# Kernel tuning notes

Hardware: AMD Instinct MI355X
Metric: run time of the kernel (lower is better)

## Reference

```python
import jax, jax.numpy as jnp
import numpy as np

N_MODES = 64


def setup_inputs() -> dict:
    key = jax.random.key(0)
    ks = jax.random.split(key, 5)
    B, L, C, M = 32, 8192, 64, N_MODES
    scale = 1.0 / (C * M)
    return {
        "x": jax.random.normal(ks[0], (B, L, C), dtype=jnp.float32),
        "w_spec_real": jax.random.normal(ks[1], (C, C, M), dtype=jnp.float32) * scale,
        "w_spec_imag": jax.random.normal(ks[2], (C, C, M), dtype=jnp.float32) * scale,
        "pw_weight": jax.random.normal(ks[3], (C, C), dtype=jnp.float32) * (1.0 / np.sqrt(C)),
        "pw_bias": jax.random.normal(ks[4], (C,), dtype=jnp.float32) * 0.01,
    }


def reference(x, w_spec_real, w_spec_imag, pw_weight, pw_bias):
    # x: [B, L, C] -> [B, C, L] (matches torch transpose(1, 2))
    xt = jnp.swapaxes(x, 1, 2)
    L = xt.shape[-1]
    xf = jnp.fft.rfft(xt, axis=-1)            # [B, C, F] complex64, F = L//2 + 1
    F = xf.shape[-1]
    K = min(N_MODES, F)
    W = (w_spec_real + 1j * w_spec_imag).astype(xf.dtype)  # [Cin, Cout, M]
    # Batched replacement of the per-mode loop: [B,Cin,K] x [Cin,Cout,K] -> [B,Cout,K]
    tf_low = jnp.einsum('bik,iok->bok', xf[:, :, :K], W[:, :, :K])
    tf = jnp.zeros_like(xf).at[:, :, :K].set(tf_low)
    x_back = jnp.fft.irfft(tf, n=L, axis=-1)  # [B, C, L] real
    # pointwise conv (kernel_size=1): [Cout,Cin] x [B,Cin,L] + bias
    pw = jnp.einsum('oi,bil->bol', pw_weight, xt) + pw_bias[None, :, None]
    return jnp.swapaxes(x_back + pw, 1, 2)     # [B, L, C]
```

## Files before the change

### kernel.cpp

```cpp
#include <hip/hip_runtime.h>
#include <stdint.h>

#define L_     8192
#define NB     32
#define NC     64
#define SPLITK 16
#define CHUNK  (L_ / SPLITK)
#define SXPAD  520

#define BF_OFF  0
#define XF_OFF  (2u  << 20)
#define XR_OFF  (18u << 20)
#define TF_OFF  (19u << 20)

typedef __bf16 bf16x8 __attribute__((ext_vector_type(8)));
typedef float  f32x4  __attribute__((ext_vector_type(4)));

__device__ __forceinline__ unsigned short f2bf(float f) {
  union { float f; unsigned int i; } v; v.f = f;
  unsigned int r = v.i + 0x7fffu + ((v.i >> 16) & 1u);
  return (unsigned short)(r >> 16);
}
__device__ __forceinline__ f32x4 mfma16(bf16x8 a, bf16x8 b, f32x4 c) {
  return __builtin_amdgcn_mfma_f32_16x16x32_bf16(a, b, c, 0, 0, 0);
}

__global__ __launch_bounds__(256) void k0_bf(unsigned short* __restrict__ Bf) {
  const int e0 = (blockIdx.x * 256 + threadIdx.x) * 4;
  const float W0 = 6.283185307179586f / 8192.0f;
  #pragma unroll
  for (int u = 0; u < 4; ++u) {
    const int e = e0 + u;
    const int j = e >> 13, l = e & 8191, k = j >> 1;
    const float th = (float)((k * l) & 8191) * W0;
    float sv, cv; __sincosf(th, &sv, &cv);
    const float a = (k == 0 ? 1.0f : 2.0f) * (1.0f / 8192.0f);
    Bf[e] = f2bf((j & 1) ? (-a * sv) : (a * cv));
  }
}

__global__ __launch_bounds__(256) void k1_dft(const float* __restrict__ x,
                                              const unsigned short* __restrict__ Bf,
                                              float* __restrict__ XFP) {
  const int b = blockIdx.x >> 4;
  const int p = blockIdx.x & 15;
  const int l0 = p * CHUNK;
  const int t = threadIdx.x;
  const int wv = t >> 6, lane = t & 63, q = lane >> 4, n = lane & 15;
  __shared__ uint32_t sx[NC * SXPAD / 2];
  const float* xb = x + (size_t)b * L_ * NC;

  {
    const int g  = t & 15;
    const int r2 = t >> 4;
    for (int s = 0; s < 16; ++s) {
      const int lrow = s * 32 + 2 * r2;
      const f32x4 u0 = *(const f32x4*)(xb + (size_t)(l0 + lrow) * NC + 4 * g);
      const f32x4 u1 = *(const f32x4*)(xb + (size_t)(l0 + lrow + 1) * NC + 4 * g);
      #pragma unroll
      for (int j = 0; j < 4; ++j) {
        __bf16 pk2[2] = {(__bf16)u0[j], (__bf16)u1[j]};
        sx[(4 * g + j) * (SXPAD / 2) + s * 16 + r2] = __builtin_bit_cast(uint32_t, pk2);
      }
    }
  }
  __syncthreads();

  f32x4 acc[2][4];
  #pragma unroll
  for (int i = 0; i < 2; ++i)
    #pragma unroll
    for (int j = 0; j < 4; ++j) acc[i][j] = (f32x4){0.f, 0.f, 0.f, 0.f};
  const unsigned short* sxu = (const unsigned short*)sx;

  for (int ks = 0; ks < CHUNK; ks += 32) {
    const int lb = ks + q * 8;
    bf16x8 bfr[4];
    #pragma unroll
    for (int nt = 0; nt < 4; ++nt)
      bfr[nt] = *(const bf16x8*)(sxu + (nt * 16 + n) * SXPAD + lb);
    #pragma unroll
    for (int mt = 0; mt < 2; ++mt) {
      const bf16x8 afr = *(const bf16x8*)(Bf + (size_t)(wv * 32 + mt * 16 + n) * L_ + l0 + lb);
      #pragma unroll
      for (int nt = 0; nt < 4; ++nt)
        acc[mt][nt] = mfma16(afr, bfr[nt], acc[mt][nt]);
    }
  }

  float* op = XFP + (size_t)(p * NB + b) * 8192;
  #pragma unroll
  for (int mt = 0; mt < 2; ++mt)
    #pragma unroll
    for (int nt = 0; nt < 4; ++nt)
      #pragma unroll
      for (int r = 0; r < 4; ++r)
        op[(wv * 32 + mt * 16 + q * 4 + r) * 64 + nt * 16 + n] = acc[mt][nt][r];
}

__global__ __launch_bounds__(256) void k1b_red(const f32x4* __restrict__ XFP,
                                               f32x4* __restrict__ XFR) {
  const int idx = blockIdx.x * 256 + threadIdx.x;
  f32x4 s = XFP[idx];
  #pragma unroll
  for (int p = 1; p < SPLITK; ++p) {
    const f32x4 v = XFP[(size_t)p * 65536 + idx];
    s[0] += v[0]; s[1] += v[1]; s[2] += v[2]; s[3] += v[3];
  }
  XFR[idx] = s;
}

__global__ __launch_bounds__(256) void k2_mix(const float* __restrict__ XFR,
                                              const float* __restrict__ wr,
                                              const float* __restrict__ wi,
                                              const float* __restrict__ pww,
                                              uint32_t* __restrict__ tf_stage) {
  const int b = blockIdx.x >> 3;
  const int og = blockIdx.x & 7;
  const int t = threadIdx.x;
  __shared__ float sxr[64 * 65];
  __shared__ float sxi[64 * 65];
  const float* xfb = XFR + (size_t)b * 8192;
  for (int e = t; e < 8192; e += 256) {
    const float s = xfb[e];
    const int j = e >> 6, c = e & 63, m = j >> 1;
    if (j & 1) sxi[c * 65 + m] = s; else sxr[c * 65 + m] = s;
  }
  __syncthreads();
  const int k = t & 63;
  const int wv = t >> 6;
  #pragma unroll
  for (int oo = 0; oo < 2; ++oo) {
    const int o = og * 8 + wv * 2 + oo;
    float ar = 0.f, ai = 0.f;
    #pragma unroll 8
    for (int i = 0; i < 64; ++i) {
      const float xr  = sxr[i * 65 + k];
      const float xi_ = sxi[i * 65 + k];
      const float wrv = wr[(size_t)i * 4096 + o * 64 + k];
      const float wiv = wi[(size_t)i * 4096 + o * 64 + k];
      ar = fmaf(xr, wrv, ar);  ar = fmaf(-xi_, wiv, ar);
      ai = fmaf(xr, wiv, ai);  ai = fmaf(xi_, wrv, ai);
    }
    uint32_t* row = tf_stage + ((size_t)b * 64 + o) * 96;
    row[k] = (uint32_t)f2bf(ar) | ((uint32_t)f2bf(ai) << 16);
    if (k < 32)
      row[64 + k] = (uint32_t)f2bf(pww[o * 64 + 2 * k]) |
                    ((uint32_t)f2bf(pww[o * 64 + 2 * k + 1]) << 16);
  }
}

__global__ __launch_bounds__(256) void k2b_copy(const uint4* __restrict__ src,
                                                uint4* __restrict__ dst) {
  const int idx = blockIdx.x * 256 + threadIdx.x;
  dst[idx] = src[idx];
}

__global__ __launch_bounds__(256) void k3_out(const float* __restrict__ x,
                                              const unsigned short* __restrict__ tf,
                                              const float* __restrict__ bias,
                                              float* __restrict__ out) {
  const int b = blockIdx.x >> 6;
  const int lt = blockIdx.x & 63;
  const int wv = threadIdx.x >> 6;
  const int lane = threadIdx.x & 63;
  const int q = lane >> 4;
  const int n = lane & 15;
  const int l0 = lt * 128 + wv * 32;
  const float* xb = x + (size_t)b * L_ * NC;
  const unsigned short* tfb = tf + (size_t)b * 64 * 192;
  const float W0 = 6.283185307179586f / 8192.0f;
  f32x4 acc[2][4];
  #pragma unroll
  for (int i = 0; i < 2; ++i)
    #pragma unroll
    for (int j = 0; j < 4; ++j) acc[i][j] = (f32x4){0.f, 0.f, 0.f, 0.f};
  const int la  = l0 + n;
  const int lb2 = l0 + 16 + n;
  #pragma unroll
  for (int s = 0; s < 6; ++s) {
    const int k0 = s * 32;
    bf16x8 a0, a1;
    if (s < 4) {
      #pragma unroll
      for (int jj = 0; jj < 4; ++jj) {
        const int kf = (k0 >> 1) + q * 4 + jj;
        float sv, cv;
        __sincosf((float)((kf * la) & 8191) * W0, &sv, &cv);
        a0[2 * jj] = (__bf16)cv; a0[2 * jj + 1] = (__bf16)(-sv);
        __sincosf((float)((kf * lb2) & 8191) * W0, &sv, &cv);
        a1[2 * jj] = (__bf16)cv; a1[2 * jj + 1] = (__bf16)(-sv);
      }
    } else {
      const int cc = (k0 - 128) + q * 8;
      const f32x4* p0 = (const f32x4*)(xb + (size_t)la  * NC + cc);
      const f32x4* p1 = (const f32x4*)(xb + (size_t)lb2 * NC + cc);
      const f32x4 u00 = p0[0], u01 = p0[1], u10 = p1[0], u11 = p1[1];
      #pragma unroll
      for (int j = 0; j < 4; ++j) {
        a0[j] = (__bf16)u00[j]; a0[4 + j] = (__bf16)u01[j];
        a1[j] = (__bf16)u10[j]; a1[4 + j] = (__bf16)u11[j];
      }
    }
    #pragma unroll
    for (int nt = 0; nt < 4; ++nt) {
      const bf16x8 bfrag = *(const bf16x8*)(tfb + (size_t)(nt * 16 + n) * 192 + k0 + q * 8);
      acc[0][nt] = mfma16(a0, bfrag, acc[0][nt]);
      acc[1][nt] = mfma16(a1, bfrag, acc[1][nt]);
    }
  }
  float* ob = out + (size_t)b * L_ * NC;
  #pragma unroll
  for (int nt = 0; nt < 4; ++nt) {
    const float bv = bias[nt * 16 + n];
    #pragma unroll
    for (int mt = 0; mt < 2; ++mt)
      #pragma unroll
      for (int r = 0; r < 4; ++r) {
        const int row = l0 + mt * 16 + q * 4 + r;
        ob[(size_t)row * NC + nt * 16 + n] = acc[mt][nt][r] + bv;
      }
  }
}

extern "C" void kernel_launch(void* const* d_in, const int* in_sizes, int n_in,
                              void* d_out, int out_size, void* d_ws, size_t ws_size,
                              hipStream_t stream) {
  (void)in_sizes; (void)n_in; (void)out_size; (void)d_ws; (void)ws_size;
  const float* x    = (const float*)d_in[0];
  float*       wr   = (float*)d_in[1];
  const float* wi   = (const float*)d_in[2];
  const float* pww  = (const float*)d_in[3];
  const float* bias = (const float*)d_in[4];
  float* out = (float*)d_out;

  char* ob = (char*)d_out;
  unsigned short* Bf  = (unsigned short*)(ob + BF_OFF);
  float*          XFP = (float*)(ob + XF_OFF);
  float*          XFR = (float*)(ob + XR_OFF);
  uint32_t*       TFS = (uint32_t*)(ob + TF_OFF);

  k0_bf   <<<1024,        256, 0, stream>>>(Bf);
  k1_dft  <<<NB * SPLITK, 256, 0, stream>>>(x, Bf, XFP);
  k1b_red <<<256,         256, 0, stream>>>((const f32x4*)XFP, (f32x4*)XFR);
  k2_mix  <<<NB * 8,      256, 0, stream>>>(XFR, wr, wi, pww, TFS);
  k2b_copy<<<192,         256, 0, stream>>>((const uint4*)TFS, (uint4*)wr);
  k3_out  <<<NB * 64,     256, 0, stream>>>(x, (const unsigned short*)wr, bias, out);
}
```

Before: 174.9 us.

## Vectorize stores, split DFT channels, transpose MFMA roles, drop mix staging

k0 now writes eight bf16 basis values per thread as a single 16-byte store. k1 splits each block's channels into two halves, doubling the grid and halving LDS, and writes its partial spectra in a channel-major layout using vector stores. k2 drops the LDS transpose and reads the interleaved real/imag spectrum directly, using twice as many blocks with one output channel per wave. k3 swaps the MFMA operand roles so each lane holds four consecutive output channels and the bias add and output writes become 16-byte vector stores. Together these aim to cut scattered scalar global stores and raise occupancy, in exchange for reloading Bf in k1 twice per chunk.

```diff
diff --git a/kernel.cpp b/kernel.cpp
--- a/kernel.cpp
+++ b/kernel.cpp
@@ -26,65 +26,69 @@
 }
 
 __global__ __launch_bounds__(256) void k0_bf(unsigned short* __restrict__ Bf) {
-  const int e0 = (blockIdx.x * 256 + threadIdx.x) * 4;
+  const int e0 = (blockIdx.x * 256 + threadIdx.x) * 8;
+  const int j = e0 >> 13, l0 = e0 & 8191, k = j >> 1;
   const float W0 = 6.283185307179586f / 8192.0f;
+  const float a = (k == 0 ? 1.0f : 2.0f) * (1.0f / 8192.0f);
+  uint32_t w[4];
   #pragma unroll
   for (int u = 0; u < 4; ++u) {
-    const int e = e0 + u;
-    const int j = e >> 13, l = e & 8191, k = j >> 1;
-    const float th = (float)((k * l) & 8191) * W0;
-    float sv, cv; __sincosf(th, &sv, &cv);
-    const float a = (k == 0 ? 1.0f : 2.0f) * (1.0f / 8192.0f);
-    Bf[e] = f2bf((j & 1) ? (-a * sv) : (a * cv));
-  }
+    float s0, c0, s1, c1;
+    __sincosf((float)((k * (l0 + 2 * u)) & 8191) * W0, &s0, &c0);
+    __sincosf((float)((k * (l0 + 2 * u + 1)) & 8191) * W0, &s1, &c1);
+    const unsigned short b0 = f2bf((j & 1) ? (-a * s0) : (a * c0));
+    const unsigned short b1 = f2bf((j & 1) ? (-a * s1) : (a * c1));
+    w[u] = (uint32_t)b0 | ((uint32_t)b1 << 16);
+  }
+  uint4 v; v.x = w[0]; v.y = w[1]; v.z = w[2]; v.w = w[3];
+  *(uint4*)(Bf + e0) = v;
 }
 
 __global__ __launch_bounds__(256) void k1_dft(const float* __restrict__ x,
                                               const unsigned short* __restrict__ Bf,
                                               float* __restrict__ XFP) {
-  const int b = blockIdx.x >> 4;
-  const int p = blockIdx.x & 15;
+  const int b = blockIdx.x >> 5;
+  const int p = (blockIdx.x >> 1) & 15;
+  const int h = blockIdx.x & 1;
   const int l0 = p * CHUNK;
   const int t = threadIdx.x;
   const int wv = t >> 6, lane = t & 63, q = lane >> 4, n = lane & 15;
-  __shared__ uint32_t sx[NC * SXPAD / 2];
-  const float* xb = x + (size_t)b * L_ * NC;
+  __shared__ uint32_t sx[32 * (SXPAD / 2)];
+  const float* xb = x + (size_t)b * L_ * NC + h * 32;
 
   {
-    const int g  = t & 15;
-    const int r2 = t >> 4;
-    for (int s = 0; s < 16; ++s) {
-      const int lrow = s * 32 + 2 * r2;
-      const f32x4 u0 = *(const f32x4*)(xb + (size_t)(l0 + lrow) * NC + 4 * g);
-      const f32x4 u1 = *(const f32x4*)(xb + (size_t)(l0 + lrow + 1) * NC + 4 * g);
+    const int g  = t & 7;
+    const int r2 = t >> 3;
+    #pragma unroll
+    for (int s = 0; s < 8; ++s) {
+      const int lp = s * 32 + r2;
+      const f32x4 u0 = *(const f32x4*)(xb + (size_t)(l0 + 2 * lp) * NC + 4 * g);
+      const f32x4 u1 = *(const f32x4*)(xb + (size_t)(l0 + 2 * lp + 1) * NC + 4 * g);
       #pragma unroll
-      for (int j = 0; j < 4; ++j) {
-        __bf16 pk2[2] = {(__bf16)u0[j], (__bf16)u1[j]};
-        sx[(4 * g + j) * (SXPAD / 2) + s * 16 + r2] = __builtin_bit_cast(uint32_t, pk2);
+      for (int jj = 0; jj < 4; ++jj) {
+        __bf16 pk2[2] = {(__bf16)u0[jj], (__bf16)u1[jj]};
+        sx[(4 * g + jj) * (SXPAD / 2) + lp] = __builtin_bit_cast(uint32_t, pk2);
       }
     }
   }
   __syncthreads();
 
-  f32x4 acc[2][4];
+  f32x4 acc[2][2];
   #pragma unroll
   for (int i = 0; i < 2; ++i)
     #pragma unroll
-    for (int j = 0; j < 4; ++j) acc[i][j] = (f32x4){0.f, 0.f, 0.f, 0.f};
+    for (int jn = 0; jn < 2; ++jn) acc[i][jn] = (f32x4){0.f, 0.f, 0.f, 0.f};
   const unsigned short* sxu = (const unsigned short*)sx;
 
   for (int ks = 0; ks < CHUNK; ks += 32) {
     const int lb = ks + q * 8;
-    bf16x8 bfr[4];
-    #pragma unroll
-    for (int nt = 0; nt < 4; ++nt)
-      bfr[nt] = *(const bf16x8*)(sxu + (nt * 16 + n) * SXPAD + lb);
+    const bf16x8 bfr0 = *(const bf16x8*)(sxu + (n)      * SXPAD + lb);
+    const bf16x8 bfr1 = *(const bf16x8*)(sxu + (16 + n) * SXPAD + lb);
     #pragma unroll
     for (int mt = 0; mt < 2; ++mt) {
       const bf16x8 afr = *(const bf16x8*)(Bf + (size_t)(wv * 32 + mt * 16 + n) * L_ + l0 + lb);
-      #pragma unroll
-      for (int nt = 0; nt < 4; ++nt)
-        acc[mt][nt] = mfma16(afr, bfr[nt], acc[mt][nt]);
+      acc[mt][0] = mfma16(afr, bfr0, acc[mt][0]);
+      acc[mt][1] = mfma16(afr, bfr1, acc[mt][1]);
     }
   }
 
@@ -92,10 +96,9 @@
   #pragma unroll
   for (int mt = 0; mt < 2; ++mt)
     #pragma unroll
-    for (int nt = 0; nt < 4; ++nt)
-      #pragma unroll
-      for (int r = 0; r < 4; ++r)
-        op[(wv * 32 + mt * 16 + q * 4 + r) * 64 + nt * 16 + n] = acc[mt][nt][r];
+    for (int nt = 0; nt < 2; ++nt)
+      *(f32x4*)(op + (size_t)(h * 32 + nt * 16 + n) * 128 + (wv * 32 + mt * 16 + q * 4)) =
+          acc[mt][nt];
 }
 
 __global__ __launch_bounds__(256) void k1b_red(const f32x4* __restrict__ XFP,
@@ -115,39 +118,27 @@
                                               const float* __restrict__ wi,
                                               const float* __restrict__ pww,
                                               uint32_t* __restrict__ tf_stage) {
-  const int b = blockIdx.x >> 3;
-  const int og = blockIdx.x & 7;
+  const int b = blockIdx.x >> 4;
+  const int og = blockIdx.x & 15;
   const int t = threadIdx.x;
-  __shared__ float sxr[64 * 65];
-  __shared__ float sxi[64 * 65];
-  const float* xfb = XFR + (size_t)b * 8192;
-  for (int e = t; e < 8192; e += 256) {
-    const float s = xfb[e];
-    const int j = e >> 6, c = e & 63, m = j >> 1;
-    if (j & 1) sxi[c * 65 + m] = s; else sxr[c * 65 + m] = s;
-  }
-  __syncthreads();
   const int k = t & 63;
   const int wv = t >> 6;
-  #pragma unroll
-  for (int oo = 0; oo < 2; ++oo) {
-    const int o = og * 8 + wv * 2 + oo;
-    float ar = 0.f, ai = 0.f;
-    #pragma unroll 8
-    for (int i = 0; i < 64; ++i) {
-      const float xr  = sxr[i * 65 + k];
-      const float xi_ = sxi[i * 65 + k];
-      const float wrv = wr[(size_t)i * 4096 + o * 64 + k];
-      const float wiv = wi[(size_t)i * 4096 + o * 64 + k];
-      ar = fmaf(xr, wrv, ar);  ar = fmaf(-xi_, wiv, ar);
-      ai = fmaf(xr, wiv, ai);  ai = fmaf(xi_, wrv, ai);
-    }
-    uint32_t* row = tf_stage + ((size_t)b * 64 + o) * 96;
-    row[k] = (uint32_t)f2bf(ar) | ((uint32_t)f2bf(ai) << 16);
-    if (k < 32)
-      row[64 + k] = (uint32_t)f2bf(pww[o * 64 + 2 * k]) |
-                    ((uint32_t)f2bf(pww[o * 64 + 2 * k + 1]) << 16);
-  }
+  const int o = og * 4 + wv;
+  const float2* xfb = (const float2*)(XFR + (size_t)b * 8192);
+  float ar = 0.f, ai = 0.f;
+  #pragma unroll 8
+  for (int i = 0; i < 64; ++i) {
+    const float2 xv  = xfb[i * 64 + k];
+    const float  wrv = wr[(size_t)i * 4096 + o * 64 + k];
+    const float  wiv = wi[(size_t)i * 4096 + o * 64 + k];
+    ar = fmaf(xv.x, wrv, ar);  ar = fmaf(-xv.y, wiv, ar);
+    ai = fmaf(xv.x, wiv, ai);  ai = fmaf(xv.y, wrv, ai);
+  }
+  uint32_t* row = tf_stage + ((size_t)b * 64 + o) * 96;
+  row[k] = (uint32_t)f2bf(ar) | ((uint32_t)f2bf(ai) << 16);
+  if (k < 32)
+    row[64 + k] = (uint32_t)f2bf(pww[o * 64 + 2 * k]) |
+                  ((uint32_t)f2bf(pww[o * 64 + 2 * k + 1]) << 16);
 }
 
 __global__ __launch_bounds__(256) void k2b_copy(const uint4* __restrict__ src,
@@ -170,56 +161,56 @@
   const float* xb = x + (size_t)b * L_ * NC;
   const unsigned short* tfb = tf + (size_t)b * 64 * 192;
   const float W0 = 6.283185307179586f / 8192.0f;
-  f32x4 acc[2][4];
-  #pragma unroll
-  for (int i = 0; i < 2; ++i)
-    #pragma unroll
-    for (int j = 0; j < 4; ++j) acc[i][j] = (f32x4){0.f, 0.f, 0.f, 0.f};
-  const int la  = l0 + n;
-  const int lb2 = l0 + 16 + n;
+  f32x4 acc[4][2];
+  #pragma unroll
+  for (int i = 0; i < 4; ++i)
+    #pragma unroll
+    for (int jn = 0; jn < 2; ++jn) acc[i][jn] = (f32x4){0.f, 0.f, 0.f, 0.f};
+  const int lA = l0 + n;
+  const int lB = l0 + 16 + n;
   #pragma unroll
   for (int s = 0; s < 6; ++s) {
     const int k0 = s * 32;
-    bf16x8 a0, a1;
+    bf16x8 b0, b1;
     if (s < 4) {
       #pragma unroll
       for (int jj = 0; jj < 4; ++jj) {
         const int kf = (k0 >> 1) + q * 4 + jj;
         float sv, cv;
-        __sincosf((float)((kf * la) & 8191) * W0, &sv, &cv);
-        a0[2 * jj] = (__bf16)cv; a0[2 * jj + 1] = (__bf16)(-sv);
-        __sincosf((float)((kf * lb2) & 8191) * W0, &sv, &cv);
-        a1[2 * jj] = (__bf16)cv; a1[2 * jj + 1] = (__bf16)(-sv);
+        __sincosf((float)((kf * lA) & 8191) * W0, &sv, &cv);
+        b0[2 * jj] = (__bf16)cv; b0[2 * jj + 1] = (__bf16)(-sv);
+        __sincosf((float)((kf * lB) & 8191) * W0, &sv, &cv);
+        b1[2 * jj] = (__bf16)cv; b1[2 * jj + 1] = (__bf16)(-sv);
       }
     } else {
       const int cc = (k0 - 128) + q * 8;
-      const f32x4* p0 = (const f32x4*)(xb + (size_t)la  * NC + cc);
-      const f32x4* p1 = (const f32x4*)(xb + (size_t)lb2 * NC + cc);
+      const f32x4* p0 = (const f32x4*)(xb + (size_t)lA * NC + cc);
+      const f32x4* p1 = (const f32x4*)(xb + (size_t)lB * NC + cc);
       const f32x4 u00 = p0[0], u01 = p0[1], u10 = p1[0], u11 = p1[1];
       #pragma unroll
-      for (int j = 0; j < 4; ++j) {
-        a0[j] = (__bf16)u00[j]; a0[4 + j] = (__bf16)u01[j];
-        a1[j] = (__bf16)u10[j]; a1[4 + j] = (__bf16)u11[j];
+      for (int jj = 0; jj < 4; ++jj) {
+        b0[jj] = (__bf16)u00[jj]; b0[4 + jj] = (__bf16)u01[jj];
+        b1[jj] = (__bf16)u10[jj]; b1[4 + jj] = (__bf16)u11[jj];
       }
     }
     #pragma unroll
-    for (int nt = 0; nt < 4; ++nt) {
-      const bf16x8 bfrag = *(const bf16x8*)(tfb + (size_t)(nt * 16 + n) * 192 + k0 + q * 8);
-      acc[0][nt] = mfma16(a0, bfrag, acc[0][nt]);
-      acc[1][nt] = mfma16(a1, bfrag, acc[1][nt]);
+    for (int mt = 0; mt < 4; ++mt) {
+      const bf16x8 afr = *(const bf16x8*)(tfb + (size_t)(mt * 16 + n) * 192 + k0 + q * 8);
+      acc[mt][0] = mfma16(afr, b0, acc[mt][0]);
+      acc[mt][1] = mfma16(afr, b1, acc[mt][1]);
     }
   }
   float* ob = out + (size_t)b * L_ * NC;
   #pragma unroll
-  for (int nt = 0; nt < 4; ++nt) {
-    const float bv = bias[nt * 16 + n];
-    #pragma unroll
-    for (int mt = 0; mt < 2; ++mt)
-      #pragma unroll
-      for (int r = 0; r < 4; ++r) {
-        const int row = l0 + mt * 16 + q * 4 + r;
-        ob[(size_t)row * NC + nt * 16 + n] = acc[mt][nt][r] + bv;
-      }
+  for (int mt = 0; mt < 4; ++mt) {
+    const f32x4 bv = *(const f32x4*)(bias + mt * 16 + q * 4);
+    #pragma unroll
+    for (int nt = 0; nt < 2; ++nt) {
+      const int l = l0 + nt * 16 + n;
+      f32x4 v = acc[mt][nt];
+      v[0] += bv[0]; v[1] += bv[1]; v[2] += bv[2]; v[3] += bv[3];
+      *(f32x4*)(ob + (size_t)l * NC + mt * 16 + q * 4) = v;
+    }
   }
 }
 
@@ -240,10 +231,10 @@
   float*          XFR = (float*)(ob + XR_OFF);
   uint32_t*       TFS = (uint32_t*)(ob + TF_OFF);
 
-  k0_bf   <<<1024,        256, 0, stream>>>(Bf);
-  k1_dft  <<<NB * SPLITK, 256, 0, stream>>>(x, Bf, XFP);
-  k1b_red <<<256,         256, 0, stream>>>((const f32x4*)XFP, (f32x4*)XFR);
-  k2_mix  <<<NB * 8,      256, 0, stream>>>(XFR, wr, wi, pww, TFS);
-  k2b_copy<<<192,         256, 0, stream>>>((const uint4*)TFS, (uint4*)wr);
-  k3_out  <<<NB * 64,     256, 0, stream>>>(x, (const unsigned short*)wr, bias, out);
-}
+  k0_bf   <<<512,             256, 0, stream>>>(Bf);
+  k1_dft  <<<NB * SPLITK * 2, 256, 0, stream>>>(x, Bf, XFP);
+  k1b_red <<<256,             256, 0, stream>>>((const f32x4*)XFP, (f32x4*)XFR);
+  k2_mix  <<<NB * 16,         256, 0, stream>>>(XFR, wr, wi, pww, TFS);
+  k2b_copy<<<192,             256, 0, stream>>>((const uint4*)TFS, (uint4*)wr);
+  k3_out  <<<NB * 64,         256, 0, stream>>>(x, (const unsigned short*)wr, bias, out);
+}
```

Measured after the change: 200.9 us. 1.15x slower.
